# Kernel optimization log

Measured on AMD Instinct MI355X. Metric: run time of the kernel, lower is better.

## Reference

```python
import jax, jax.numpy as jnp
import numpy as np

N_NODES = 50000
N_EDGES = 800000
D_IN = 512
D_OUT = 128

def setup_inputs() -> dict:
    key = jax.random.key(0)
    k1, k2, k3, k4, k5, k6 = jax.random.split(key, 6)
    std = 1.0 / np.sqrt(D_OUT)
    x = jax.random.normal(k1, (N_NODES, D_IN), dtype=jnp.float32)
    edge_w = jax.random.uniform(k2, (N_EDGES,), dtype=jnp.float32)
    src = jax.random.randint(k3, (N_EDGES,), 0, N_NODES, dtype=jnp.int32)
    dst = jax.random.randint(k4, (N_EDGES,), 0, N_NODES, dtype=jnp.int32)
    W = jax.random.uniform(k5, (D_IN, D_OUT), minval=-std, maxval=std, dtype=jnp.float32)
    b = jax.random.uniform(k6, (D_OUT,), minval=-std, maxval=std, dtype=jnp.float32)
    return {"x": x, "edge_w": edge_w, "src": src, "dst": dst, "W": W, "b": b}

def reference(x, edge_w, src, dst, W, b):
    # Dense GEMM: [N, D_in] @ [D_in, D_out]
    h = x @ W
    # SpMM with COO adjacency: out[i] = sum_{e: dst[e]==i} edge_w[e] * h[src[e]]
    msg = h[src] * edge_w[:, None]          # [E, D_out]
    agg = jax.ops.segment_sum(msg, dst, num_segments=N_NODES)
    return agg + b
```

## Files before the change

kernel.cpp:

```cpp
#include <hip/hip_runtime.h>
#include <hip/hip_bf16.h>

#define M_NODES  50000
#define D_IN_K   512
#define D_OUT_N  128
#define N_EDGES  800000
#define SCAN_NBLK 49

typedef short  bf16x8 __attribute__((ext_vector_type(8)));
typedef float  f32x4  __attribute__((ext_vector_type(4)));

static __device__ __forceinline__ unsigned short f2bf(float f) {
    unsigned u = __float_as_uint(f);
    unsigned r = u + 0x7FFF + ((u >> 16) & 1);
    return (unsigned short)(r >> 16);
}
static __device__ __forceinline__ float bflo(unsigned q) { return __uint_as_float(q << 16); }
static __device__ __forceinline__ float bfhi(unsigned q) { return __uint_as_float(q & 0xFFFF0000u); }

__global__ __launch_bounds__(256) void setup_kernel(const float* __restrict__ W,
                                                    unsigned short* __restrict__ Wp,
                                                    int* __restrict__ counts) {
    if (blockIdx.x < 32) {
        int tid = blockIdx.x * 256 + threadIdx.x;
        int lane = tid & 63;
        int nt   = (tid >> 6) & 7;
        int kb4  = tid >> 9;
        int n    = nt * 16 + (lane & 15);
        int kbase = kb4 * 32 + ((lane >> 4) & 3) * 8;
        unsigned short frag[8];
#pragma unroll
        for (int j = 0; j < 8; ++j)
            frag[j] = f2bf(W[(size_t)(kbase + j) * D_OUT_N + n]);
        *(uint4*)&Wp[(size_t)tid * 8] = *(const uint4*)frag;
    } else {
        int i = (blockIdx.x - 32) * 256 + threadIdx.x;
        if (i < M_NODES) counts[i] = 0;
    }
}

__global__ __launch_bounds__(256, 2) void mfma_gemm_kernel(const float* __restrict__ x,
                                                           const uint4* __restrict__ Wp4,
                                                           unsigned short* __restrict__ h) {
    __shared__ uint4 wlds[4096];

    const int wave = threadIdx.x >> 6;
    const int lane = threadIdx.x & 63;
    const int m0   = blockIdx.x * 128 + wave * 32;
    const int mrow = lane & 15;
    const int kgrp = lane >> 4;

    const int r0 = m0 + mrow;
    const int r1 = m0 + 16 + mrow;
    const float* xr0 = x + (size_t)((r0 < M_NODES) ? r0 : M_NODES - 1) * D_IN_K + kgrp * 8;
    const float* xr1 = x + (size_t)((r1 < M_NODES) ? r1 : M_NODES - 1) * D_IN_K + kgrp * 8;

    f32x4 acc[2][8];
#pragma unroll
    for (int f = 0; f < 2; ++f)
#pragma unroll
        for (int t = 0; t < 8; ++t) acc[f][t] = (f32x4){0.f, 0.f, 0.f, 0.f};

    for (int half = 0; half < 2; ++half) {
        __syncthreads();
#pragma unroll
        for (int i = 0; i < 16; ++i)
            wlds[threadIdx.x + i * 256] = Wp4[half * 4096 + threadIdx.x + i * 256];
        __syncthreads();

        const float* px0 = xr0 + half * 256;
        const float* px1 = xr1 + half * 256;

        float4 a00 = *(const float4*)(px0);
        float4 a01 = *(const float4*)(px0 + 4);
        float4 a10 = *(const float4*)(px1);
        float4 a11 = *(const float4*)(px1 + 4);

#pragma unroll
        for (int kb = 0; kb < 8; ++kb) {
            float4 n00, n01, n10, n11;
            if (kb < 7) {
                n00 = *(const float4*)(px0 + (kb + 1) * 32);
                n01 = *(const float4*)(px0 + (kb + 1) * 32 + 4);
                n10 = *(const float4*)(px1 + (kb + 1) * 32);
                n11 = *(const float4*)(px1 + (kb + 1) * 32 + 4);
            }

            union { bf16x8 v; __hip_bfloat162 h2[4]; } c0, c1;
            c0.h2[0] = __float22bfloat162_rn(make_float2(a00.x, a00.y));
            c0.h2[1] = __float22bfloat162_rn(make_float2(a00.z, a00.w));
            c0.h2[2] = __float22bfloat162_rn(make_float2(a01.x, a01.y));
            c0.h2[3] = __float22bfloat162_rn(make_float2(a01.z, a01.w));
            c1.h2[0] = __float22bfloat162_rn(make_float2(a10.x, a10.y));
            c1.h2[1] = __float22bfloat162_rn(make_float2(a10.z, a10.w));
            c1.h2[2] = __float22bfloat162_rn(make_float2(a11.x, a11.y));
            c1.h2[3] = __float22bfloat162_rn(make_float2(a11.z, a11.w));
            bf16x8 a0 = c0.v, a1 = c1.v;

#pragma unroll
            for (int nt = 0; nt < 8; ++nt) {
                union { uint4 u; bf16x8 v; } wb;
                wb.u = wlds[(kb * 8 + nt) * 64 + lane];
                acc[0][nt] = __builtin_amdgcn_mfma_f32_16x16x32_bf16(a0, wb.v, acc[0][nt], 0, 0, 0);
                acc[1][nt] = __builtin_amdgcn_mfma_f32_16x16x32_bf16(a1, wb.v, acc[1][nt], 0, 0, 0);
            }

            if (kb < 7) { a00 = n00; a01 = n01; a10 = n10; a11 = n11; }
        }
    }

#pragma unroll
    for (int f = 0; f < 2; ++f)
#pragma unroll
        for (int r = 0; r < 4; ++r) {
            int rr = m0 + f * 16 + kgrp * 4 + r;
            if (rr < M_NODES) {
                unsigned short* hp = h + (size_t)rr * D_OUT_N + mrow;
#pragma unroll
                for (int nt = 0; nt < 8; ++nt)
                    hp[nt * 16] = f2bf(acc[f][nt][r]);
            }
        }
}

__global__ __launch_bounds__(256) void hist_kernel(const int* __restrict__ dst,
                                                   int* __restrict__ counts) {
    int e = blockIdx.x * blockDim.x + threadIdx.x;
    if (e < N_EDGES) atomicAdd(&counts[dst[e]], 1);
}

__global__ __launch_bounds__(256) void scan_partial_kernel(const int* __restrict__ counts,
                                                           int* __restrict__ offsets,
                                                           int* __restrict__ partials) {
    __shared__ int wsum[4];
    const int tid  = threadIdx.x;
    const int lane = tid & 63;
    const int wid  = tid >> 6;
    const int base = blockIdx.x * 1024 + tid * 4;

    int v[4];
#pragma unroll
    for (int i = 0; i < 4; ++i) v[i] = (base + i < M_NODES) ? counts[base + i] : 0;
    int t = v[0] + v[1] + v[2] + v[3];

    int s = t;
#pragma unroll
    for (int d = 1; d < 64; d <<= 1) {
        int u = __shfl_up(s, d, 64);
        if (lane >= d) s += u;
    }
    if (lane == 63) wsum[wid] = s;
    __syncthreads();
    int wbase = 0;
#pragma unroll
    for (int w = 0; w < 4; ++w) wbase += (w < wid) ? wsum[w] : 0;

    int run = wbase + s - t;
#pragma unroll
    for (int i = 0; i < 4; ++i) {
        if (base + i < M_NODES) offsets[base + i] = run;
        run += v[i];
    }
    if (tid == 255) partials[blockIdx.x] = wbase + s;
}

__global__ __launch_bounds__(64) void scan_carry_kernel(const int* __restrict__ partials,
                                                        int* __restrict__ carries,
                                                        int* __restrict__ offsets) {
    int lane = threadIdx.x;
    int v = (lane < SCAN_NBLK) ? partials[lane] : 0;
    int s = v;
#pragma unroll
    for (int d = 1; d < 64; d <<= 1) {
        int u = __shfl_up(s, d, 64);
        if (lane >= d) s += u;
    }
    if (lane < SCAN_NBLK) carries[lane] = s - v;
    if (lane == 63) offsets[M_NODES] = s;
}

__global__ __launch_bounds__(256) void scan_add_kernel(int* __restrict__ offsets,
                                                       const int* __restrict__ carries,
                                                       int* __restrict__ cursor) {
    const int base = blockIdx.x * 1024 + threadIdx.x * 4;
    const int c = carries[blockIdx.x];
#pragma unroll
    for (int i = 0; i < 4; ++i) {
        if (base + i < M_NODES) {
            int o = offsets[base + i] + c;
            offsets[base + i] = o;
            cursor[base + i] = o;
        }
    }
}

__global__ __launch_bounds__(256) void fill_kernel(const int* __restrict__ src,
                                                   const int* __restrict__ dst,
                                                   const float* __restrict__ edge_w,
                                                   int* __restrict__ cursor,
                                                   int2* __restrict__ ep) {
    int e = blockIdx.x * blockDim.x + threadIdx.x;
    if (e >= N_EDGES) return;
    int d   = dst[e];
    int pos = atomicAdd(&cursor[d], 1);
    ep[pos] = make_int2(src[e], __float_as_int(edge_w[e]));
}

__global__ __launch_bounds__(256) void gather_kernel(const unsigned short* __restrict__ h,
                                                     const int2* __restrict__ ep,
                                                     const int* __restrict__ offsets,
                                                     const float* __restrict__ b,
                                                     float* __restrict__ out) {
    int t    = blockIdx.x * blockDim.x + threadIdx.x;
    int node = t >> 4;
    int lane = t & 15;
    if (node >= M_NODES) return;
    int beg = offsets[node];
    int end = offsets[node + 1];

    float4 b0 = *(const float4*)&b[lane * 8];
    float4 b1 = *(const float4*)&b[lane * 8 + 4];
    float a[4][8];
#pragma unroll
    for (int u = 0; u < 4; ++u)
#pragma unroll
        for (int c = 0; c < 8; ++c) a[u][c] = 0.f;

    int j = beg;
    for (; j + 4 <= end; j += 4) {
        int2 e0 = ep[j], e1 = ep[j + 1], e2 = ep[j + 2], e3 = ep[j + 3];
        uint4 q0 = *(const uint4*)(h + (size_t)e0.x * D_OUT_N + lane * 8);
        uint4 q1 = *(const uint4*)(h + (size_t)e1.x * D_OUT_N + lane * 8);
        uint4 q2 = *(const uint4*)(h + (size_t)e2.x * D_OUT_N + lane * 8);
        uint4 q3 = *(const uint4*)(h + (size_t)e3.x * D_OUT_N + lane * 8);
        float w0 = __int_as_float(e0.y), w1 = __int_as_float(e1.y);
        float w2 = __int_as_float(e2.y), w3 = __int_as_float(e3.y);
        a[0][0] += w0 * bflo(q0.x);  a[0][1] += w0 * bfhi(q0.x);
        a[0][2] += w0 * bflo(q0.y);  a[0][3] += w0 * bfhi(q0.y);
        a[0][4] += w0 * bflo(q0.z);  a[0][5] += w0 * bfhi(q0.z);
        a[0][6] += w0 * bflo(q0.w);  a[0][7] += w0 * bfhi(q0.w);
        a[1][0] += w1 * bflo(q1.x);  a[1][1] += w1 * bfhi(q1.x);
        a[1][2] += w1 * bflo(q1.y);  a[1][3] += w1 * bfhi(q1.y);
        a[1][4] += w1 * bflo(q1.z);  a[1][5] += w1 * bfhi(q1.z);
        a[1][6] += w1 * bflo(q1.w);  a[1][7] += w1 * bfhi(q1.w);
        a[2][0] += w2 * bflo(q2.x);  a[2][1] += w2 * bfhi(q2.x);
        a[2][2] += w2 * bflo(q2.y);  a[2][3] += w2 * bfhi(q2.y);
        a[2][4] += w2 * bflo(q2.z);  a[2][5] += w2 * bfhi(q2.z);
        a[2][6] += w2 * bflo(q2.w);  a[2][7] += w2 * bfhi(q2.w);
        a[3][0] += w3 * bflo(q3.x);  a[3][1] += w3 * bfhi(q3.x);
        a[3][2] += w3 * bflo(q3.y);  a[3][3] += w3 * bfhi(q3.y);
        a[3][4] += w3 * bflo(q3.z);  a[3][5] += w3 * bfhi(q3.z);
        a[3][6] += w3 * bflo(q3.w);  a[3][7] += w3 * bfhi(q3.w);
    }
    for (; j < end; ++j) {
        int2 e0 = ep[j];
        float w0 = __int_as_float(e0.y);
        uint4 q0 = *(const uint4*)(h + (size_t)e0.x * D_OUT_N + lane * 8);
        a[0][0] += w0 * bflo(q0.x);  a[0][1] += w0 * bfhi(q0.x);
        a[0][2] += w0 * bflo(q0.y);  a[0][3] += w0 * bfhi(q0.y);
        a[0][4] += w0 * bflo(q0.z);  a[0][5] += w0 * bfhi(q0.z);
        a[0][6] += w0 * bflo(q0.w);  a[0][7] += w0 * bfhi(q0.w);
    }

    float4 o0 = make_float4(b0.x + a[0][0] + a[1][0] + a[2][0] + a[3][0],
                            b0.y + a[0][1] + a[1][1] + a[2][1] + a[3][1],
                            b0.z + a[0][2] + a[1][2] + a[2][2] + a[3][2],
                            b0.w + a[0][3] + a[1][3] + a[2][3] + a[3][3]);
    float4 o1 = make_float4(b1.x + a[0][4] + a[1][4] + a[2][4] + a[3][4],
                            b1.y + a[0][5] + a[1][5] + a[2][5] + a[3][5],
                            b1.z + a[0][6] + a[1][6] + a[2][6] + a[3][6],
                            b1.w + a[0][7] + a[1][7] + a[2][7] + a[3][7]);
    float* op = &out[(size_t)node * D_OUT_N + lane * 8];
    *(float4*)op = o0;
    *(float4*)(op + 4) = o1;
}

extern "C" void kernel_launch(void* const* d_in, const int* in_sizes, int n_in,
                              void* d_out, int out_size, void* d_ws, size_t ws_size,
                              hipStream_t stream) {
    const float* x      = (const float*)d_in[0];
    const float* edge_w = (const float*)d_in[1];
    const int*   src    = (const int*)d_in[2];
    const int*   dst    = (const int*)d_in[3];
    const float* W      = (const float*)d_in[4];
    const float* b      = (const float*)d_in[5];
    float* out = (float*)d_out;

    char* wsp = (char*)d_ws;
    unsigned short* h = (unsigned short*)wsp;  wsp += (size_t)M_NODES * D_OUT_N * 2;
    int*   counts   = (int*)wsp;         wsp += ((size_t)M_NODES * 4 + 15) & ~15ull;
    int*   offsets  = (int*)wsp;         wsp += (((size_t)M_NODES + 1) * 4 + 15) & ~15ull;
    int*   cursor   = (int*)wsp;         wsp += ((size_t)M_NODES * 4 + 15) & ~15ull;
    int2*  ep       = (int2*)wsp;        wsp += (size_t)N_EDGES * 8;
    unsigned short* Wp = (unsigned short*)wsp; wsp += (size_t)16 * 8 * 64 * 8 * 2;
    int*   partials = (int*)wsp;         wsp += (SCAN_NBLK * 4 + 15) & ~15ull;
    int*   carries  = (int*)wsp;         wsp += (SCAN_NBLK * 4 + 15) & ~15ull;

    setup_kernel<<<32 + (M_NODES + 255) / 256, 256, 0, stream>>>(W, Wp, counts);
    mfma_gemm_kernel<<<(M_NODES + 127) / 128, 256, 0, stream>>>(x, (const uint4*)Wp, h);
    hist_kernel<<<(N_EDGES + 255) / 256, 256, 0, stream>>>(dst, counts);
    scan_partial_kernel<<<SCAN_NBLK, 256, 0, stream>>>(counts, offsets, partials);
    scan_carry_kernel<<<1, 64, 0, stream>>>(partials, carries, offsets);
    scan_add_kernel<<<SCAN_NBLK, 256, 0, stream>>>(offsets, carries, cursor);
    fill_kernel<<<(N_EDGES + 255) / 256, 256, 0, stream>>>(src, dst, edge_w, cursor, ep);
    gather_kernel<<<(int)(((long long)M_NODES * 16 + 255) / 256), 256, 0, stream>>>(
        h, ep, offsets, b, out);
}
```

Measured before the change: 297.3 us.

## Fuse histogram into GEMM, single-pass scan, and pad atomic counters

Appends the dst-degree histogram to the tail of the GEMM kernel and replaces the three scan kernels with one decoupled-lookback scan that spins on per-block flags. Counters and cursors are strided by 16 ints so each atomic target sits on its own cache line. Zeroing moves to a hipMemsetAsync. This cuts kernel launches and is meant to reduce atomic contention, in exchange for a larger memset and the lookback scan's reliance on all 49 blocks being co-resident.

```diff
diff --git a/kernel.cpp b/kernel.cpp
--- a/kernel.cpp
+++ b/kernel.cpp
@@ -6,6 +6,7 @@
 #define D_OUT_N  128
 #define N_EDGES  800000
 #define SCAN_NBLK 49
+#define PAD 16
 
 typedef short  bf16x8 __attribute__((ext_vector_type(8)));
 typedef float  f32x4  __attribute__((ext_vector_type(4)));
@@ -18,30 +19,26 @@
 static __device__ __forceinline__ float bflo(unsigned q) { return __uint_as_float(q << 16); }
 static __device__ __forceinline__ float bfhi(unsigned q) { return __uint_as_float(q & 0xFFFF0000u); }
 
-__global__ __launch_bounds__(256) void setup_kernel(const float* __restrict__ W,
-                                                    unsigned short* __restrict__ Wp,
-                                                    int* __restrict__ counts) {
-    if (blockIdx.x < 32) {
-        int tid = blockIdx.x * 256 + threadIdx.x;
-        int lane = tid & 63;
-        int nt   = (tid >> 6) & 7;
-        int kb4  = tid >> 9;
-        int n    = nt * 16 + (lane & 15);
-        int kbase = kb4 * 32 + ((lane >> 4) & 3) * 8;
-        unsigned short frag[8];
-#pragma unroll
-        for (int j = 0; j < 8; ++j)
-            frag[j] = f2bf(W[(size_t)(kbase + j) * D_OUT_N + n]);
-        *(uint4*)&Wp[(size_t)tid * 8] = *(const uint4*)frag;
-    } else {
-        int i = (blockIdx.x - 32) * 256 + threadIdx.x;
-        if (i < M_NODES) counts[i] = 0;
-    }
-}
-
-__global__ __launch_bounds__(256, 2) void mfma_gemm_kernel(const float* __restrict__ x,
-                                                           const uint4* __restrict__ Wp4,
-                                                           unsigned short* __restrict__ h) {
+__global__ __launch_bounds__(256) void permw_kernel(const float* __restrict__ W,
+                                                    unsigned short* __restrict__ Wp) {
+    int tid = blockIdx.x * 256 + threadIdx.x;
+    int lane = tid & 63;
+    int nt   = (tid >> 6) & 7;
+    int kb4  = tid >> 9;
+    int n    = nt * 16 + (lane & 15);
+    int kbase = kb4 * 32 + ((lane >> 4) & 3) * 8;
+    unsigned short frag[8];
+#pragma unroll
+    for (int j = 0; j < 8; ++j)
+        frag[j] = f2bf(W[(size_t)(kbase + j) * D_OUT_N + n]);
+    *(uint4*)&Wp[(size_t)tid * 8] = *(const uint4*)frag;
+}
+
+__global__ __launch_bounds__(256, 2) void mfma_gemm_hist_kernel(const float* __restrict__ x,
+                                                                const uint4* __restrict__ Wp4,
+                                                                unsigned short* __restrict__ h,
+                                                                const int* __restrict__ dst,
+                                                                int* __restrict__ counts) {
     __shared__ uint4 wlds[4096];
 
     const int wave = threadIdx.x >> 6;
@@ -121,26 +118,31 @@
                     hp[nt * 16] = f2bf(acc[f][nt][r]);
             }
         }
-}
-
-__global__ __launch_bounds__(256) void hist_kernel(const int* __restrict__ dst,
-                                                   int* __restrict__ counts) {
-    int e = blockIdx.x * blockDim.x + threadIdx.x;
-    if (e < N_EDGES) atomicAdd(&counts[dst[e]], 1);
-}
-
-__global__ __launch_bounds__(256) void scan_partial_kernel(const int* __restrict__ counts,
-                                                           int* __restrict__ offsets,
-                                                           int* __restrict__ partials) {
+
+    const int epb = (N_EDGES + gridDim.x - 1) / gridDim.x;
+    const int e0  = blockIdx.x * epb;
+    const int e1  = (e0 + epb < N_EDGES) ? e0 + epb : N_EDGES;
+    for (int e = e0 + threadIdx.x; e < e1; e += 256)
+        atomicAdd(&counts[dst[e] * PAD], 1);
+}
+
+__global__ __launch_bounds__(256) void scan_kernel(const int* __restrict__ counts,
+                                                   int* __restrict__ offsets,
+                                                   int* __restrict__ cursor,
+                                                   int* __restrict__ partials,
+                                                   int* __restrict__ flags) {
     __shared__ int wsum[4];
+    __shared__ int carry_s;
     const int tid  = threadIdx.x;
     const int lane = tid & 63;
     const int wid  = tid >> 6;
-    const int base = blockIdx.x * 1024 + tid * 4;
+    const int blk  = blockIdx.x;
+    const int base = blk * 1024 + tid * 4;
 
     int v[4];
 #pragma unroll
-    for (int i = 0; i < 4; ++i) v[i] = (base + i < M_NODES) ? counts[base + i] : 0;
+    for (int i = 0; i < 4; ++i)
+        v[i] = (base + i < M_NODES) ? counts[(base + i) * PAD] : 0;
     int t = v[0] + v[1] + v[2] + v[3];
 
     int s = t;
@@ -154,43 +156,35 @@
     int wbase = 0;
 #pragma unroll
     for (int w = 0; w < 4; ++w) wbase += (w < wid) ? wsum[w] : 0;
-
-    int run = wbase + s - t;
-#pragma unroll
-    for (int i = 0; i < 4; ++i) {
-        if (base + i < M_NODES) offsets[base + i] = run;
-        run += v[i];
-    }
-    if (tid == 255) partials[blockIdx.x] = wbase + s;
-}
-
-__global__ __launch_bounds__(64) void scan_carry_kernel(const int* __restrict__ partials,
-                                                        int* __restrict__ carries,
-                                                        int* __restrict__ offsets) {
-    int lane = threadIdx.x;
-    int v = (lane < SCAN_NBLK) ? partials[lane] : 0;
-    int s = v;
-#pragma unroll
-    for (int d = 1; d < 64; d <<= 1) {
-        int u = __shfl_up(s, d, 64);
-        if (lane >= d) s += u;
-    }
-    if (lane < SCAN_NBLK) carries[lane] = s - v;
-    if (lane == 63) offsets[M_NODES] = s;
-}
-
-__global__ __launch_bounds__(256) void scan_add_kernel(int* __restrict__ offsets,
-                                                       const int* __restrict__ carries,
-                                                       int* __restrict__ cursor) {
-    const int base = blockIdx.x * 1024 + threadIdx.x * 4;
-    const int c = carries[blockIdx.x];
+    int total = wsum[0] + wsum[1] + wsum[2] + wsum[3];
+
+    if (tid == 0) {
+        __hip_atomic_store(&partials[blk], total, __ATOMIC_RELAXED, __HIP_MEMORY_SCOPE_AGENT);
+        __hip_atomic_store(&flags[blk], 1, __ATOMIC_RELEASE, __HIP_MEMORY_SCOPE_AGENT);
+        if (blk == 0) offsets[M_NODES] = N_EDGES;
+    }
+
+    if (wid == 0) {
+        int val = 0;
+        if (lane < blk) {
+            while (__hip_atomic_load(&flags[lane], __ATOMIC_ACQUIRE, __HIP_MEMORY_SCOPE_AGENT) == 0) {}
+            val = __hip_atomic_load(&partials[lane], __ATOMIC_RELAXED, __HIP_MEMORY_SCOPE_AGENT);
+        }
+#pragma unroll
+        for (int d = 32; d > 0; d >>= 1) val += __shfl_xor(val, d, 64);
+        if (lane == 0) carry_s = val;
+    }
+    __syncthreads();
+    const int carry = carry_s;
+
+    int run = carry + wbase + s - t;
 #pragma unroll
     for (int i = 0; i < 4; ++i) {
         if (base + i < M_NODES) {
-            int o = offsets[base + i] + c;
-            offsets[base + i] = o;
-            cursor[base + i] = o;
+            offsets[base + i] = run;
+            cursor[(base + i) * PAD] = run;
         }
+        run += v[i];
     }
 }
 
@@ -202,7 +196,7 @@
     int e = blockIdx.x * blockDim.x + threadIdx.x;
     if (e >= N_EDGES) return;
     int d   = dst[e];
-    int pos = atomicAdd(&cursor[d], 1);
+    int pos = atomicAdd(&cursor[d * PAD], 1);
     ep[pos] = make_int2(src[e], __float_as_int(edge_w[e]));
 }
 
@@ -288,20 +282,19 @@
 
     char* wsp = (char*)d_ws;
     unsigned short* h = (unsigned short*)wsp;  wsp += (size_t)M_NODES * D_OUT_N * 2;
-    int*   counts   = (int*)wsp;         wsp += ((size_t)M_NODES * 4 + 15) & ~15ull;
+    int*   counts   = (int*)wsp;         wsp += (size_t)M_NODES * PAD * 4;
+    int*   flags    = (int*)wsp;         wsp += 64 * 4;
+    int*   cursor   = (int*)wsp;         wsp += (size_t)M_NODES * PAD * 4;
     int*   offsets  = (int*)wsp;         wsp += (((size_t)M_NODES + 1) * 4 + 15) & ~15ull;
-    int*   cursor   = (int*)wsp;         wsp += ((size_t)M_NODES * 4 + 15) & ~15ull;
     int2*  ep       = (int2*)wsp;        wsp += (size_t)N_EDGES * 8;
     unsigned short* Wp = (unsigned short*)wsp; wsp += (size_t)16 * 8 * 64 * 8 * 2;
     int*   partials = (int*)wsp;         wsp += (SCAN_NBLK * 4 + 15) & ~15ull;
-    int*   carries  = (int*)wsp;         wsp += (SCAN_NBLK * 4 + 15) & ~15ull;
-
-    setup_kernel<<<32 + (M_NODES + 255) / 256, 256, 0, stream>>>(W, Wp, counts);
-    mfma_gemm_kernel<<<(M_NODES + 127) / 128, 256, 0, stream>>>(x, (const uint4*)Wp, h);
-    hist_kernel<<<(N_EDGES + 255) / 256, 256, 0, stream>>>(dst, counts);
-    scan_partial_kernel<<<SCAN_NBLK, 256, 0, stream>>>(counts, offsets, partials);
-    scan_carry_kernel<<<1, 64, 0, stream>>>(partials, carries, offsets);
-    scan_add_kernel<<<SCAN_NBLK, 256, 0, stream>>>(offsets, carries, cursor);
+
+    hipMemsetAsync(counts, 0, (size_t)M_NODES * PAD * 4 + 64 * 4, stream);
+    permw_kernel<<<32, 256, 0, stream>>>(W, Wp);
+    mfma_gemm_hist_kernel<<<(M_NODES + 127) / 128, 256, 0, stream>>>(
+        x, (const uint4*)Wp, h, dst, counts);
+    scan_kernel<<<SCAN_NBLK, 256, 0, stream>>>(counts, offsets, cursor, partials, flags);
     fill_kernel<<<(N_EDGES + 255) / 256, 256, 0, stream>>>(src, dst, edge_w, cursor, ep);
     gather_kernel<<<(int)(((long long)M_NODES * 16 + 255) / 256), 256, 0, stream>>>(
         h, ep, offsets, b, out);
```

Result: no change. 291.9 us (-1.8%).
